# Optimization experiments

Measured on AMD Instinct MI355X. Metric: run time of the kernel, lower is better.

Reference implementation:

```python
import jax, jax.numpy as jnp
import numpy as np

NS, NW, E, DIN, OUT, H = 100_000, 400_000, 500_000, 64, 64, 4


def setup_inputs() -> dict:
    key = jax.random.key(0)
    ks = jax.random.split(key, 26)
    s = 1.0 / np.sqrt(DIN)
    sg = 1.0 / np.sqrt(OUT)
    inp = {
        "x_sites": jax.random.normal(ks[0], (NS, DIN), jnp.float32),
        "x_wells": jax.random.normal(ks[1], (NW, DIN), jnp.float32),
        "edge_sw_src": jax.random.randint(ks[2], (E,), 0, NS, jnp.int32),
        "edge_sw_dst": jax.random.randint(ks[3], (E,), 0, NW, jnp.int32),
        "edge_ws_src": jax.random.randint(ks[4], (E,), 0, NW, jnp.int32),
        "edge_ws_dst": jax.random.randint(ks[5], (E,), 0, NS, jnp.int32),
        # GAT ('pfas_sites','distance','gw_wells'), heads=4, concat=False
        "W_sw": jax.random.normal(ks[6], (DIN, H * OUT), jnp.float32) * s,
        "att_src_sw": jax.random.normal(ks[7], (H, OUT), jnp.float32) * sg,
        "att_dst_sw": jax.random.normal(ks[8], (H, OUT), jnp.float32) * sg,
        "b_sw": jnp.zeros((OUT,), jnp.float32),
        # SAGE ('gw_wells','distance','pfas_sites')
        "Wl_ws": jax.random.normal(ks[9], (DIN, OUT), jnp.float32) * s,
        "bl_ws": jnp.zeros((OUT,), jnp.float32),
        "Wr_ws": jax.random.normal(ks[10], (DIN, OUT), jnp.float32) * s,
        # GAT ('pfas_sites','self_loop','pfas_sites'), add_self_loops=True -> identity edges
        "W_ss": jax.random.normal(ks[11], (DIN, H * OUT), jnp.float32) * s,
        "att_src_ss": jax.random.normal(ks[12], (H, OUT), jnp.float32) * sg,
        "att_dst_ss": jax.random.normal(ks[13], (H, OUT), jnp.float32) * sg,
        "b_ss": jnp.zeros((OUT,), jnp.float32),
        # SAGE ('gw_wells','self_loop','gw_wells') with identity edges
        "Wl_ww": jax.random.normal(ks[14], (DIN, OUT), jnp.float32) * s,
        "bl_ww": jnp.zeros((OUT,), jnp.float32),
        "Wr_ww": jax.random.normal(ks[15], (DIN, OUT), jnp.float32) * s,
        # output heads
        "Wg": jax.random.normal(ks[16], (OUT, 1), jnp.float32) * sg,
        "bg": jnp.zeros((1,), jnp.float32),
        "Wsit": jax.random.normal(ks[17], (OUT, 1), jnp.float32) * sg,
        "bsit": jnp.zeros((1,), jnp.float32),
    }
    return inp


def _gat(x_src, x_dst, src, dst, W, a_src, a_dst, b, n_dst):
    """PyG GATConv, concat=False (mean over heads), negative_slope=0.2."""
    h, c = a_src.shape
    xs = (x_src @ W).reshape(-1, h, c)  # [Ns,H,C]
    xd = (x_dst @ W).reshape(-1, h, c)  # [Nd,H,C]
    al_s = jnp.einsum("nhc,hc->nh", xs, a_src)
    al_d = jnp.einsum("nhc,hc->nh", xd, a_dst)
    e = jax.nn.leaky_relu(al_s[src] + al_d[dst], 0.2)  # [E,H]
    m = jax.ops.segment_max(e, dst, num_segments=n_dst)
    ex = jnp.exp(e - m[dst])
    denom = jax.ops.segment_sum(ex, dst, num_segments=n_dst)
    alpha = ex / denom[dst]  # edge-softmax per dst node
    msg = xs[src] * alpha[:, :, None]  # [E,H,C] dominant intermediate
    out = jax.ops.segment_sum(msg, dst, num_segments=n_dst)
    return out.mean(axis=1) + b


def _sage(x_src, x_dst, src, dst, Wl, bl, Wr, n_dst):
    """PyG SAGEConv, mean aggregation, root_weight=True."""
    ssum = jax.ops.segment_sum(x_src[src], dst, num_segments=n_dst)
    cnt = jax.ops.segment_sum(jnp.ones((src.shape[0],), x_src.dtype), dst, num_segments=n_dst)
    mean = ssum / jnp.maximum(cnt, 1.0)[:, None]  # empty neighborhood -> 0 (PyG mean scatter)
    return mean @ Wl + bl + x_dst @ Wr


def reference(x_sites, x_wells, edge_sw_src, edge_sw_dst, edge_ws_src, edge_ws_dst,
              W_sw, att_src_sw, att_dst_sw, b_sw, Wl_ws, bl_ws, Wr_ws,
              W_ss, att_src_ss, att_dst_ss, b_ss, Wl_ww, bl_ww, Wr_ww,
              Wg, bg, Wsit, bsit):
    # relation 1: GAT sites -> wells
    gw = _gat(x_sites, x_wells, edge_sw_src, edge_sw_dst, W_sw, att_src_sw, att_dst_sw, b_sw, NW)
    # relation 4: SAGE self-loop on wells; identity edges -> mean == x itself
    gw = gw + (x_wells @ Wl_ww + bl_ww + x_wells @ Wr_ww)  # HeteroConv aggr='sum'
    # relation 2: SAGE wells -> sites
    si = _sage(x_wells, x_sites, edge_ws_src, edge_ws_dst, Wl_ws, bl_ws, Wr_ws, NS)
    # relation 3: GAT self-loop on sites (add_self_loops=True -> identity edge set);
    # softmax over a single self edge is 1, so output = mean over heads of lin(x) + bias
    si = si + (x_sites @ W_ss).reshape(NS, H, OUT).mean(axis=1) + b_ss
    # post: relu -> dropout (eval mode: identity) -> linear -> leaky_relu(0.01)
    gw = jax.nn.relu(gw)
    si = jax.nn.relu(si)
    o_gw = jax.nn.leaky_relu(gw @ Wg + bg, 0.01)   # [NW, 1]
    o_si = jax.nn.leaky_relu(si @ Wsit + bsit, 0.01)  # [NS, 1]
    return o_gw, o_si
```

## Files before the change

### kernel.cpp

```cpp
#include <hip/hip_runtime.h>

#define NS_ 100000
#define NW_ 400000
#define NE_ 500000
#define EPB 2048

typedef float f32x4_t __attribute__((ext_vector_type(4)));
typedef unsigned u32x4_t __attribute__((ext_vector_type(4)));

__device__ __forceinline__ float lrelu02(float x) { return x > 0.f ? x : 0.2f * x; }
__device__ __forceinline__ float bf2f(unsigned short u) {
    return __uint_as_float(((unsigned)u) << 16);
}
__device__ __forceinline__ unsigned short f2bf(float f) {
    unsigned u = __float_as_uint(f);
    u += 0x7FFFu + ((u >> 16) & 1u);
    return (unsigned short)(u >> 16);
}
__device__ __forceinline__ unsigned pk(float lo, float hi) {
    return (unsigned)f2bf(lo) | ((unsigned)f2bf(hi) << 16);
}
__device__ __forceinline__ void mfma_bf16(f32x4_t& acc, u32x4_t a, u32x4_t b) {
    asm volatile("v_mfma_f32_16x16x32_bf16 %0, %1, %2, %0" : "+v"(acc) : "v"(a), "v"(b));
}

__global__ void __launch_bounds__(256)
k_prep(const float* __restrict__ W_sw, const float* __restrict__ att_src,
       const float* __restrict__ att_dst,
       const float* __restrict__ Wl_ww, const float* __restrict__ Wr_ww,
       const float* __restrict__ Wl_ws, const float* __restrict__ Wr_ws,
       const float* __restrict__ W_ss,
       float* __restrict__ vd, float* __restrict__ vs,
       u32x4_t* __restrict__ fw, u32x4_t* __restrict__ fs,
       u32x4_t* __restrict__ fsp)
{
    const int tid = threadIdx.x;
    {
        int d = tid >> 2, h = tid & 3;
        const float4* wp = (const float4*)(W_sw + d * 256 + h * 64);
        const float4* ad = (const float4*)(att_dst + h * 64);
        const float4* as = (const float4*)(att_src + h * 64);
        float accd = 0.f, accs = 0.f;
#pragma unroll
        for (int c = 0; c < 16; ++c) {
            float4 wv = wp[c]; float4 dv = ad[c]; float4 sv = as[c];
            accd += wv.x * dv.x + wv.y * dv.y + wv.z * dv.z + wv.w * dv.w;
            accs += wv.x * sv.x + wv.y * sv.y + wv.z * sv.z + wv.w * sv.w;
        }
        vd[d * 4 + h] = accd;
        vs[d * 4 + h] = accs;
    }
    for (int idx = tid; idx < 512; idx += 256) {
        int f = idx >> 6, lane = idx & 63;
        int kc = f >> 2, ct = f & 3, q = lane >> 4, n = lane & 15;
        int c = ct * 16 + n;
        u32x4_t d;
#pragma unroll
        for (int i = 0; i < 4; ++i) {
            int k = kc * 32 + q * 8 + 2 * i;
            d[i] = pk(Wl_ww[k * 64 + c] + Wr_ww[k * 64 + c],
                      Wl_ww[(k + 1) * 64 + c] + Wr_ww[(k + 1) * 64 + c]);
        }
        fw[idx] = d;
    }
    for (int idx = tid; idx < 1024; idx += 256) {
        int f = idx >> 6, lane = idx & 63;
        int kc = f >> 2, ct = f & 3, q = lane >> 4, n = lane & 15;
        int c = ct * 16 + n;
        u32x4_t d;
#pragma unroll
        for (int i = 0; i < 4; ++i) {
            int k = kc * 32 + q * 8 + 2 * i;
            float lo, hi;
            if (k < 64) {
                lo = Wl_ws[k * 64 + c];
                hi = Wl_ws[(k + 1) * 64 + c];
            } else {
                int kk = k - 64;
                lo = Wr_ws[kk * 64 + c] + 0.25f * (W_ss[kk * 256 + c] + W_ss[kk * 256 + 64 + c] +
                                                   W_ss[kk * 256 + 128 + c] + W_ss[kk * 256 + 192 + c]);
                hi = Wr_ws[(kk + 1) * 64 + c] + 0.25f * (W_ss[(kk + 1) * 256 + c] + W_ss[(kk + 1) * 256 + 64 + c] +
                                                         W_ss[(kk + 1) * 256 + 128 + c] + W_ss[(kk + 1) * 256 + 192 + c]);
            }
            d[i] = pk(lo, hi);
        }
        fs[idx] = d;
    }
    for (int idx = tid; idx < 2048; idx += 256) {
        int f = idx >> 6, lane = idx & 63;
        int kc = f >> 4, ct = f & 15, q = lane >> 4, n = lane & 15;
        int c = ct * 16 + n;
        u32x4_t d;
#pragma unroll
        for (int i = 0; i < 4; ++i) {
            int k = kc * 32 + q * 8 + 2 * i;
            d[i] = pk(W_sw[k * 256 + c], W_sw[(k + 1) * 256 + c]);
        }
        fsp[idx] = d;
    }
}

#define SP_PAD 264
__global__ void __launch_bounds__(256)
k_sites_pre(const float* __restrict__ x_sites, const u32x4_t* __restrict__ fsp,
            const float* __restrict__ vs, unsigned short* __restrict__ xs,
            float* __restrict__ al_s)
{
    __shared__ unsigned short stg[4][16 * SP_PAD];
    __shared__ float vsl[256];
    const int tid = threadIdx.x;
    vsl[tid] = vs[tid];
    __syncthreads();
    const int wave = __builtin_amdgcn_readfirstlane(tid >> 6);
    const int lane = tid & 63, q = lane >> 4, n = lane & 15;
    const int sbase = blockIdx.x * 64 + wave * 16;
    const int srow = min(sbase + n, NS_ - 1);
    const float* xr = x_sites + (size_t)srow * 64 + q * 8;
    float4 x0 = *(const float4*)(xr);
    float4 x1 = *(const float4*)(xr + 4);
    float4 x2 = *(const float4*)(xr + 32);
    float4 x3 = *(const float4*)(xr + 36);
    u32x4_t am0 = { pk(x0.x, x0.y), pk(x0.z, x0.w), pk(x1.x, x1.y), pk(x1.z, x1.w) };
    u32x4_t am1 = { pk(x2.x, x2.y), pk(x2.z, x2.w), pk(x3.x, x3.y), pk(x3.z, x3.w) };
    float pa[4];
#pragma unroll
    for (int h = 0; h < 4; ++h) {
        const float* v0 = &vsl[(q * 8) * 4 + h];
        const float* v1 = &vsl[(32 + q * 8) * 4 + h];
        pa[h] = x0.x * v0[0]  + x0.y * v0[4]  + x0.z * v0[8]  + x0.w * v0[12]
              + x1.x * v0[16] + x1.y * v0[20] + x1.z * v0[24] + x1.w * v0[28]
              + x2.x * v1[0]  + x2.y * v1[4]  + x2.z * v1[8]  + x2.w * v1[12]
              + x3.x * v1[16] + x3.y * v1[20] + x3.z * v1[24] + x3.w * v1[28];
    }
#pragma unroll
    for (int h = 0; h < 4; ++h) {
        pa[h] += __shfl_xor(pa[h], 16, 64);
        pa[h] += __shfl_xor(pa[h], 32, 64);
    }
    if (q == 0 && sbase + n < NS_)
        *(float4*)(al_s + (size_t)(sbase + n) * 4) = make_float4(pa[0], pa[1], pa[2], pa[3]);

    f32x4_t acc[16];
#pragma unroll
    for (int ct = 0; ct < 16; ++ct) acc[ct] = (f32x4_t){0, 0, 0, 0};
    asm volatile("s_nop 3" : "+v"(am0), "+v"(am1));
#pragma unroll
    for (int ct = 0; ct < 16; ++ct) mfma_bf16(acc[ct], am0, fsp[ct * 64 + lane]);
#pragma unroll
    for (int ct = 0; ct < 16; ++ct) mfma_bf16(acc[ct], am1, fsp[(16 + ct) * 64 + lane]);
    asm volatile("s_nop 7\n\ts_nop 7" ::: "memory");
    unsigned short* ss = &stg[wave][0];
#pragma unroll
    for (int ct = 0; ct < 16; ++ct)
#pragma unroll
        for (int reg = 0; reg < 4; ++reg)
            ss[(q * 4 + reg) * SP_PAD + ct * 16 + n] = f2bf(acc[ct][reg]);
    __builtin_amdgcn_s_waitcnt(0);
#pragma unroll
    for (int i = 0; i < 8; ++i) {
        int g = i * 64 + lane;
        int r = g >> 5, c = g & 31;
        if (sbase + r < NS_) {
            u32x4_t v = *(const u32x4_t*)(ss + r * SP_PAD + c * 8);
            *(u32x4_t*)(xs + (size_t)(sbase + r) * 256 + c * 8) = v;
        }
    }
}

__global__ void __launch_bounds__(256)
k_hist2(const int* __restrict__ d1, int* __restrict__ h1,
        const int* __restrict__ d2, int* __restrict__ h2)
{
    int e = blockIdx.x * 256 + threadIdx.x;
    if (e >= NE_) return;
    if (blockIdx.y == 0) atomicAdd(&h1[d1[e]], 1);
    else                 atomicAdd(&h2[d2[e]], 1);
}

__global__ void __launch_bounds__(256)
k_scan1_2(const int* __restrict__ h1, int n1, int* __restrict__ b1, int nb1,
          const int* __restrict__ h2, int n2, int* __restrict__ b2)
{
    __shared__ int red[256];
    const int tid = threadIdx.x;
    const int bx = blockIdx.x;
    const int* hist; int n; int* bsum; int blk;
    if (bx < nb1) { hist = h1; n = n1; bsum = b1; blk = bx; }
    else          { hist = h2; n = n2; bsum = b2; blk = bx - nb1; }
    int base = blk * EPB + tid * 8;
    int s = 0;
#pragma unroll
    for (int i = 0; i < 8; ++i) { int idx = base + i; if (idx < n) s += hist[idx]; }
    red[tid] = s;
    __syncthreads();
    for (int off = 128; off > 0; off >>= 1) {
        if (tid < off) red[tid] += red[tid + off];
        __syncthreads();
    }
    if (tid == 0) bsum[blk] = red[0];
}

__global__ void __launch_bounds__(256)
k_scan2_2(int* __restrict__ b1, int nb1, int* __restrict__ b2, int nb2)
{
    __shared__ int sh[256];
    const int tid = threadIdx.x;
    int* bsum = blockIdx.x == 0 ? b1 : b2;
    int nb = blockIdx.x == 0 ? nb1 : nb2;
    sh[tid] = (tid < nb) ? bsum[tid] : 0;
    __syncthreads();
    for (int off = 1; off < 256; off <<= 1) {
        int u = (tid >= off) ? sh[tid - off] : 0;
        __syncthreads();
        sh[tid] += u;
        __syncthreads();
    }
    if (tid < nb) bsum[tid] = (tid == 0) ? 0 : sh[tid - 1];
}

__global__ void __launch_bounds__(256)
k_scan3_2(const int* __restrict__ h1, int n1, const int* __restrict__ b1,
          int* __restrict__ rp1, int* __restrict__ cu1, int nb1,
          const int* __restrict__ h2, int n2, const int* __restrict__ b2,
          int* __restrict__ rp2, int* __restrict__ cu2)
{
    __shared__ int tsum[256];
    const int tid = threadIdx.x;
    const int bx = blockIdx.x;
    const int* hist; int n; const int* bsum; int* rowptr; int* cursor; int blk;
    if (bx < nb1) { hist = h1; n = n1; bsum = b1; rowptr = rp1; cursor = cu1; blk = bx; }
    else          { hist = h2; n = n2; bsum = b2; rowptr = rp2; cursor = cu2; blk = bx - nb1; }
    int base = blk * EPB + tid * 8;
    int v[8]; int s = 0;
#pragma unroll
    for (int i = 0; i < 8; ++i) {
        int idx = base + i;
        v[i] = (idx < n) ? hist[idx] : 0;
        s += v[i];
    }
    tsum[tid] = s;
    __syncthreads();
    for (int off = 1; off < 256; off <<= 1) {
        int u = (tid >= off) ? tsum[tid - off] : 0;
        __syncthreads();
        tsum[tid] += u;
        __syncthreads();
    }
    int texcl = tsum[tid] - s;
    int run = bsum[blk] + texcl;
#pragma unroll
    for (int i = 0; i < 8; ++i) {
        int idx = base + i;
        if (idx < n) { rowptr[idx] = run; cursor[idx] = run; run += v[i]; }
    }
    if (blk == 0 && tid == 0) rowptr[n] = NE_;
}

__global__ void __launch_bounds__(256)
k_scatter2(const int* __restrict__ s1, const int* __restrict__ d1,
           int* __restrict__ c1, int* __restrict__ o1,
           const int* __restrict__ s2, const int* __restrict__ d2,
           int* __restrict__ c2, int* __restrict__ o2)
{
    int e = blockIdx.x * 256 + threadIdx.x;
    if (e >= NE_) return;
    if (blockIdx.y == 0) { int p = atomicAdd(&c1[d1[e]], 1); o1[p] = s1[e]; }
    else                 { int p = atomicAdd(&c2[d2[e]], 1); o2[p] = s2[e]; }
}

__global__ void __launch_bounds__(256)
k_gat_wells(const float* __restrict__ x_wells, const float* __restrict__ vd,
            const int* __restrict__ rowptr, const int* __restrict__ csr_src,
            const float* __restrict__ al_s, const unsigned short* __restrict__ xs,
            const float* __restrict__ b_sw, const float* __restrict__ bl_ww,
            const u32x4_t* __restrict__ fw, const float* __restrict__ Wg,
            const float* __restrict__ bg, float* __restrict__ out)
{
    __shared__ float vdl[16][17];
    __shared__ float xw[16][68];
    __shared__ float dl[16][68];
    __shared__ float biasl[64];
    __shared__ float wgl[64];
    __shared__ float res[16];
    const int tid = threadIdx.x;
    vdl[tid >> 4][tid & 15] = vd[tid];
    if (tid < 64) { biasl[tid] = b_sw[tid] + bl_ww[tid]; wgl[tid] = Wg[tid]; }
    __syncthreads();
    const int wl = tid >> 4, p = tid & 15;
    const int w = blockIdx.x * 16 + wl;
    float h0, h1, h2, h3;
    {
        float4 xv = *(const float4*)(x_wells + (size_t)w * 64 + 4 * p);
        *(float4*)&xw[wl][4 * p] = xv;
        const float* vp = vdl[p];
        h0 = xv.x * vp[0] + xv.y * vp[4] + xv.z * vp[8]  + xv.w * vp[12];
        h1 = xv.x * vp[1] + xv.y * vp[5] + xv.z * vp[9]  + xv.w * vp[13];
        h2 = xv.x * vp[2] + xv.y * vp[6] + xv.z * vp[10] + xv.w * vp[14];
        h3 = xv.x * vp[3] + xv.y * vp[7] + xv.z * vp[11] + xv.w * vp[15];
    }
#pragma unroll
    for (int off = 1; off < 16; off <<= 1) {
        h0 += __shfl_xor(h0, off, 64);
        h1 += __shfl_xor(h1, off, 64);
        h2 += __shfl_xor(h2, off, 64);
        h3 += __shfl_xor(h3, off, 64);
    }
    const int r0 = rowptr[w], r1 = rowptr[w + 1];
    float den0 = 0, den1 = 0, den2 = 0, den3 = 0;
    float n0[4] = {0, 0, 0, 0}, n1[4] = {0, 0, 0, 0};
    float n2[4] = {0, 0, 0, 0}, n3[4] = {0, 0, 0, 0};
    for (int j = r0; j < r1; ++j) {
        int s = csr_src[j];
        float4 as = ((const float4*)al_s)[s];
        float e0 = __expf(lrelu02(as.x + h0));
        float e1 = __expf(lrelu02(as.y + h1));
        float e2 = __expf(lrelu02(as.z + h2));
        float e3 = __expf(lrelu02(as.w + h3));
        den0 += e0; den1 += e1; den2 += e2; den3 += e3;
        const unsigned short* xr = xs + (size_t)s * 256 + 4 * p;
        ushort4 u0 = *(const ushort4*)(xr);
        ushort4 u1 = *(const ushort4*)(xr + 64);
        ushort4 u2 = *(const ushort4*)(xr + 128);
        ushort4 u3 = *(const ushort4*)(xr + 192);
        n0[0] += e0 * bf2f(u0.x); n0[1] += e0 * bf2f(u0.y); n0[2] += e0 * bf2f(u0.z); n0[3] += e0 * bf2f(u0.w);
        n1[0] += e1 * bf2f(u1.x); n1[1] += e1 * bf2f(u1.y); n1[2] += e1 * bf2f(u1.z); n1[3] += e1 * bf2f(u1.w);
        n2[0] += e2 * bf2f(u2.x); n2[1] += e2 * bf2f(u2.y); n2[2] += e2 * bf2f(u2.z); n2[3] += e2 * bf2f(u2.w);
        n3[0] += e3 * bf2f(u3.x); n3[1] += e3 * bf2f(u3.y); n3[2] += e3 * bf2f(u3.z); n3[3] += e3 * bf2f(u3.w);
    }
    const int c0 = 4 * p;
    float tmsg[4];
    if (r1 > r0) {
        float i0 = 0.25f / den0, i1 = 0.25f / den1, i2 = 0.25f / den2, i3 = 0.25f / den3;
#pragma unroll
        for (int i = 0; i < 4; ++i)
            tmsg[i] = n0[i] * i0 + n1[i] * i1 + n2[i] * i2 + n3[i] * i3 + biasl[c0 + i];
    } else {
#pragma unroll
        for (int i = 0; i < 4; ++i) tmsg[i] = biasl[c0 + i];
    }
    __syncthreads();
    const int wave = __builtin_amdgcn_readfirstlane(tid >> 6);
    const int lane = tid & 63, q = lane >> 4, n = lane & 15;
    u32x4_t a0, a1;
#pragma unroll
    for (int i = 0; i < 4; ++i) {
        a0[i] = pk(xw[n][q * 8 + 2 * i],      xw[n][q * 8 + 2 * i + 1]);
        a1[i] = pk(xw[n][32 + q * 8 + 2 * i], xw[n][32 + q * 8 + 2 * i + 1]);
    }
    f32x4_t acc = {0, 0, 0, 0};
    asm volatile("s_nop 3" : "+v"(a0), "+v"(a1), "+v"(acc));
    mfma_bf16(acc, a0, fw[wave * 64 + lane]);
    mfma_bf16(acc, a1, fw[(4 + wave) * 64 + lane]);
    asm volatile("s_nop 7\n\ts_nop 7" : "+v"(acc));
#pragma unroll
    for (int reg = 0; reg < 4; ++reg)
        dl[q * 4 + reg][wave * 16 + n] = acc[reg];
    __syncthreads();
    float4 dv = *(const float4*)&dl[wl][c0];
    float t0 = tmsg[0] + dv.x;
    float t1 = tmsg[1] + dv.y;
    float t2 = tmsg[2] + dv.z;
    float t3 = tmsg[3] + dv.w;
    float pr = fmaxf(t0, 0.f) * wgl[c0] + fmaxf(t1, 0.f) * wgl[c0 + 1] +
               fmaxf(t2, 0.f) * wgl[c0 + 2] + fmaxf(t3, 0.f) * wgl[c0 + 3];
    pr += __shfl_xor(pr, 1, 64);
    pr += __shfl_xor(pr, 2, 64);
    pr += __shfl_xor(pr, 4, 64);
    pr += __shfl_xor(pr, 8, 64);
    if (p == 0) res[wl] = pr + bg[0];
    __syncthreads();
    if (tid < 16) {
        float v = res[tid];
        out[blockIdx.x * 16 + tid] = v > 0.f ? v : 0.01f * v;
    }
}

__global__ void __launch_bounds__(256)
k_sage_sites(const float* __restrict__ x_sites, const float* __restrict__ x_wells,
             const int* __restrict__ rowptr, const int* __restrict__ csr_src,
             const u32x4_t* __restrict__ fs, const float* __restrict__ bl_ws,
             const float* __restrict__ b_ss, const float* __restrict__ Wsit,
             const float* __restrict__ bsit, float* __restrict__ out)
{
    __shared__ float mnL[16][68];
    __shared__ float xL[16][68];
    __shared__ float dl[16][68];
    __shared__ float biasl[64];
    __shared__ float wsl[64];
    __shared__ float res[16];
    const int tid = threadIdx.x;
    if (tid < 64) { biasl[tid] = bl_ws[tid] + b_ss[tid]; wsl[tid] = Wsit[tid]; }
    const int sl = tid >> 4, p = tid & 15;
    const int s = blockIdx.x * 16 + sl;
    const int r0 = rowptr[s], r1 = rowptr[s + 1];
    float4 m4 = {0.f, 0.f, 0.f, 0.f};
    for (int j = r0; j < r1; ++j) {
        int wsrc = csr_src[j];
        float4 xv = ((const float4*)(x_wells + (size_t)wsrc * 64))[p];
        m4.x += xv.x; m4.y += xv.y; m4.z += xv.z; m4.w += xv.w;
    }
    if (r1 > r0) {
        float rc = 1.f / (float)(r1 - r0);
        m4.x *= rc; m4.y *= rc; m4.z *= rc; m4.w *= rc;
    }
    *(float4*)&mnL[sl][4 * p] = m4;
    {
        float4 xv = *(const float4*)(x_sites + (size_t)s * 64 + 4 * p);
        *(float4*)&xL[sl][4 * p] = xv;
    }
    __syncthreads();
    const int wave = __builtin_amdgcn_readfirstlane(tid >> 6);
    const int lane = tid & 63, q = lane >> 4, n = lane & 15;
    u32x4_t am0, am1, ax0, ax1;
#pragma unroll
    for (int i = 0; i < 4; ++i) {
        am0[i] = pk(mnL[n][q * 8 + 2 * i],      mnL[n][q * 8 + 2 * i + 1]);
        am1[i] = pk(mnL[n][32 + q * 8 + 2 * i], mnL[n][32 + q * 8 + 2 * i + 1]);
        ax0[i] = pk(xL[n][q * 8 + 2 * i],       xL[n][q * 8 + 2 * i + 1]);
        ax1[i] = pk(xL[n][32 + q * 8 + 2 * i],  xL[n][32 + q * 8 + 2 * i + 1]);
    }
    f32x4_t acc = {0, 0, 0, 0};
    asm volatile("s_nop 3" : "+v"(am0), "+v"(am1), "+v"(ax0), "+v"(ax1), "+v"(acc));
    mfma_bf16(acc, am0, fs[wave * 64 + lane]);
    mfma_bf16(acc, am1, fs[(4 + wave) * 64 + lane]);
    mfma_bf16(acc, ax0, fs[(8 + wave) * 64 + lane]);
    mfma_bf16(acc, ax1, fs[(12 + wave) * 64 + lane]);
    asm volatile("s_nop 7\n\ts_nop 7" : "+v"(acc));
#pragma unroll
    for (int reg = 0; reg < 4; ++reg)
        dl[q * 4 + reg][wave * 16 + n] = acc[reg];
    __syncthreads();
    const int c0 = 4 * p;
    float4 dv = *(const float4*)&dl[sl][c0];
    float t0 = dv.x + biasl[c0];
    float t1 = dv.y + biasl[c0 + 1];
    float t2 = dv.z + biasl[c0 + 2];
    float t3 = dv.w + biasl[c0 + 3];
    float pr = fmaxf(t0, 0.f) * wsl[c0] + fmaxf(t1, 0.f) * wsl[c0 + 1] +
               fmaxf(t2, 0.f) * wsl[c0 + 2] + fmaxf(t3, 0.f) * wsl[c0 + 3];
    pr += __shfl_xor(pr, 1, 64);
    pr += __shfl_xor(pr, 2, 64);
    pr += __shfl_xor(pr, 4, 64);
    pr += __shfl_xor(pr, 8, 64);
    if (p == 0) res[sl] = pr + bsit[0];
    __syncthreads();
    if (tid < 16) {
        float v = res[tid];
        out[(size_t)NW_ + blockIdx.x * 16 + tid] = v > 0.f ? v : 0.01f * v;
    }
}

extern "C" void kernel_launch(void* const* d_in, const int* in_sizes, int n_in,
                              void* d_out, int out_size, void* d_ws, size_t ws_size,
                              hipStream_t stream)
{
    const float* x_sites    = (const float*)d_in[0];
    const float* x_wells    = (const float*)d_in[1];
    const int*   e_sw_src   = (const int*)d_in[2];
    const int*   e_sw_dst   = (const int*)d_in[3];
    const int*   e_ws_src   = (const int*)d_in[4];
    const int*   e_ws_dst   = (const int*)d_in[5];
    const float* W_sw       = (const float*)d_in[6];
    const float* att_src_sw = (const float*)d_in[7];
    const float* att_dst_sw = (const float*)d_in[8];
    const float* b_sw       = (const float*)d_in[9];
    const float* Wl_ws      = (const float*)d_in[10];
    const float* bl_ws      = (const float*)d_in[11];
    const float* Wr_ws      = (const float*)d_in[12];
    const float* W_ss       = (const float*)d_in[13];
    const float* b_ss       = (const float*)d_in[16];
    const float* Wl_ww      = (const float*)d_in[17];
    const float* bl_ww      = (const float*)d_in[18];
    const float* Wr_ww      = (const float*)d_in[19];
    const float* Wg         = (const float*)d_in[20];
    const float* bg         = (const float*)d_in[21];
    const float* Wsit       = (const float*)d_in[22];
    const float* bsit       = (const float*)d_in[23];
    float* out = (float*)d_out;

    unsigned short* xs = (unsigned short*)d_ws;
    float* al_s = (float*)(xs + (size_t)NS_ * 256);
    float* vd   = al_s + (size_t)NS_ * 4;
    float* vs   = vd + 256;
    u32x4_t* fw = (u32x4_t*)(vs + 256);
    u32x4_t* fs = fw + 512;
    u32x4_t* fsp= fs + 1024;
    int* ip     = (int*)(fsp + 2048);
    int* h_sw   = ip;
    int* h_ws   = h_sw + NW_;
    int* rp_sw  = h_ws + NS_;
    int* cur_sw = rp_sw + NW_ + 4;
    int* csr_sw = cur_sw + NW_;
    int* bs_sw  = csr_sw + NE_;
    int* rp_ws  = bs_sw + 256;
    int* cur_ws = rp_ws + NS_ + 4;
    int* csr_ws = cur_ws + NS_;
    int* bs_ws  = csr_ws + NE_;

    hipMemsetAsync(h_sw, 0, (size_t)(NW_ + NS_) * sizeof(int), stream);

    const int egrid = (NE_ + 255) / 256;
    const int nb_sw = (NW_ + EPB - 1) / EPB;
    const int nb_ws = (NS_ + EPB - 1) / EPB;

    hipLaunchKernelGGL(k_hist2, dim3(egrid, 2), dim3(256), 0, stream,
                       e_sw_dst, h_sw, e_ws_dst, h_ws);
    hipLaunchKernelGGL(k_scan1_2, dim3(nb_sw + nb_ws), dim3(256), 0, stream,
                       h_sw, NW_, bs_sw, nb_sw, h_ws, NS_, bs_ws);
    hipLaunchKernelGGL(k_scan2_2, dim3(2), dim3(256), 0, stream,
                       bs_sw, nb_sw, bs_ws, nb_ws);
    hipLaunchKernelGGL(k_scan3_2, dim3(nb_sw + nb_ws), dim3(256), 0, stream,
                       h_sw, NW_, bs_sw, rp_sw, cur_sw, nb_sw,
                       h_ws, NS_, bs_ws, rp_ws, cur_ws);
    hipLaunchKernelGGL(k_scatter2, dim3(egrid, 2), dim3(256), 0, stream,
                       e_sw_src, e_sw_dst, cur_sw, csr_sw,
                       e_ws_src, e_ws_dst, cur_ws, csr_ws);

    hipLaunchKernelGGL(k_prep, dim3(1), dim3(256), 0, stream,
                       W_sw, att_src_sw, att_dst_sw, Wl_ww, Wr_ww, Wl_ws, Wr_ws, W_ss,
                       vd, vs, fw, fs, fsp);
    hipLaunchKernelGGL(k_sites_pre, dim3((NS_ + 63) / 64), dim3(256), 0, stream,
                       x_sites, fsp, vs, xs, al_s);

    hipLaunchKernelGGL(k_gat_wells, dim3(NW_ / 16), dim3(256), 0, stream,
                       x_wells, vd, rp_sw, csr_sw, al_s, xs, b_sw, bl_ww,
                       fw, Wg, bg, out);
    hipLaunchKernelGGL(k_sage_sites, dim3(NS_ / 16), dim3(256), 0, stream,
                       x_sites, x_wells, rp_ws, csr_ws, fs, bl_ws, b_ss,
                       Wsit, bsit, out);
}
```

Baseline: 468.5 us.

## Inline first two well neighbors in per-node descriptor and pack staging as bf16

Replaces the wells rowptr/cursor pair with an int4 descriptor per well (start, degree, first two source ids) filled during scatter. The GAT kernel can then issue its first two neighbor gathers up front without the dependent csr_src load. The per-site bf16 features are permuted on store so each lane reads two contiguous 16-byte vectors instead of four 8-byte ones. The LDS staging in both consumer kernels holds packed bf16, so the MFMA operand is one vector load. It costs an extra per-well counter memset, a larger descriptor array and extra scatter writes.

```diff
diff --git a/kernel.cpp b/kernel.cpp
--- a/kernel.cpp
+++ b/kernel.cpp
@@ -12,6 +12,8 @@
 __device__ __forceinline__ float bf2f(unsigned short u) {
     return __uint_as_float(((unsigned)u) << 16);
 }
+__device__ __forceinline__ float lo16(unsigned u) { return __uint_as_float(u << 16); }
+__device__ __forceinline__ float hi16(unsigned u) { return __uint_as_float(u & 0xFFFF0000u); }
 __device__ __forceinline__ unsigned short f2bf(float f) {
     unsigned u = __float_as_uint(f);
     u += 0x7FFFu + ((u >> 16) & 1u);
@@ -150,11 +152,14 @@
     for (int ct = 0; ct < 16; ++ct) mfma_bf16(acc[ct], am1, fsp[(16 + ct) * 64 + lane]);
     asm volatile("s_nop 7\n\ts_nop 7" ::: "memory");
     unsigned short* ss = &stg[wave][0];
-#pragma unroll
-    for (int ct = 0; ct < 16; ++ct)
+    const int pbase = ((n >> 2) * 16) + (n & 3);
+#pragma unroll
+    for (int ct = 0; ct < 16; ++ct) {
+        const int cidx = pbase + (ct & 3) * 64 + (ct >> 2) * 4;
 #pragma unroll
         for (int reg = 0; reg < 4; ++reg)
-            ss[(q * 4 + reg) * SP_PAD + ct * 16 + n] = f2bf(acc[ct][reg]);
+            ss[(q * 4 + reg) * SP_PAD + cidx] = f2bf(acc[ct][reg]);
+    }
     __builtin_amdgcn_s_waitcnt(0);
 #pragma unroll
     for (int i = 0; i < 8; ++i) {
@@ -220,16 +225,16 @@
 
 __global__ void __launch_bounds__(256)
 k_scan3_2(const int* __restrict__ h1, int n1, const int* __restrict__ b1,
-          int* __restrict__ rp1, int* __restrict__ cu1, int nb1,
+          int4* __restrict__ desc, int nb1,
           const int* __restrict__ h2, int n2, const int* __restrict__ b2,
           int* __restrict__ rp2, int* __restrict__ cu2)
 {
     __shared__ int tsum[256];
     const int tid = threadIdx.x;
     const int bx = blockIdx.x;
-    const int* hist; int n; const int* bsum; int* rowptr; int* cursor; int blk;
-    if (bx < nb1) { hist = h1; n = n1; bsum = b1; rowptr = rp1; cursor = cu1; blk = bx; }
-    else          { hist = h2; n = n2; bsum = b2; rowptr = rp2; cursor = cu2; blk = bx - nb1; }
+    const int* hist; int n; const int* bsum; int blk; int wells;
+    if (bx < nb1) { hist = h1; n = n1; bsum = b1; blk = bx; wells = 1; }
+    else          { hist = h2; n = n2; bsum = b2; blk = bx - nb1; wells = 0; }
     int base = blk * EPB + tid * 8;
     int v[8]; int s = 0;
 #pragma unroll
@@ -248,36 +253,52 @@
     }
     int texcl = tsum[tid] - s;
     int run = bsum[blk] + texcl;
-#pragma unroll
-    for (int i = 0; i < 8; ++i) {
-        int idx = base + i;
-        if (idx < n) { rowptr[idx] = run; cursor[idx] = run; run += v[i]; }
-    }
-    if (blk == 0 && tid == 0) rowptr[n] = NE_;
+    if (wells) {
+#pragma unroll
+        for (int i = 0; i < 8; ++i) {
+            int idx = base + i;
+            if (idx < n) { desc[idx] = make_int4(run, v[i], 0, 0); run += v[i]; }
+        }
+    } else {
+#pragma unroll
+        for (int i = 0; i < 8; ++i) {
+            int idx = base + i;
+            if (idx < n) { rp2[idx] = run; cu2[idx] = run; run += v[i]; }
+        }
+        if (blk == 0 && tid == 0) rp2[n] = NE_;
+    }
 }
 
 __global__ void __launch_bounds__(256)
 k_scatter2(const int* __restrict__ s1, const int* __restrict__ d1,
-           int* __restrict__ c1, int* __restrict__ o1,
+           int* __restrict__ cnt0, int* __restrict__ desc_i, int* __restrict__ o1,
            const int* __restrict__ s2, const int* __restrict__ d2,
            int* __restrict__ c2, int* __restrict__ o2)
 {
     int e = blockIdx.x * 256 + threadIdx.x;
     if (e >= NE_) return;
-    if (blockIdx.y == 0) { int p = atomicAdd(&c1[d1[e]], 1); o1[p] = s1[e]; }
-    else                 { int p = atomicAdd(&c2[d2[e]], 1); o2[p] = s2[e]; }
+    if (blockIdx.y == 0) {
+        int d = d1[e], s = s1[e];
+        int pr = atomicAdd(&cnt0[d], 1);
+        int start = desc_i[4 * d];
+        o1[start + pr] = s;
+        if (pr < 2) desc_i[4 * d + 2 + pr] = s;
+    } else {
+        int p = atomicAdd(&c2[d2[e]], 1);
+        o2[p] = s2[e];
+    }
 }
 
 __global__ void __launch_bounds__(256)
 k_gat_wells(const float* __restrict__ x_wells, const float* __restrict__ vd,
-            const int* __restrict__ rowptr, const int* __restrict__ csr_src,
+            const int4* __restrict__ desc, const int* __restrict__ csr_src,
             const float* __restrict__ al_s, const unsigned short* __restrict__ xs,
             const float* __restrict__ b_sw, const float* __restrict__ bl_ww,
             const u32x4_t* __restrict__ fw, const float* __restrict__ Wg,
             const float* __restrict__ bg, float* __restrict__ out)
 {
     __shared__ float vdl[16][17];
-    __shared__ float xw[16][68];
+    __shared__ unsigned xwB[16][36];
     __shared__ float dl[16][68];
     __shared__ float biasl[64];
     __shared__ float wgl[64];
@@ -288,10 +309,24 @@
     __syncthreads();
     const int wl = tid >> 4, p = tid & 15;
     const int w = blockIdx.x * 16 + wl;
+    const int4 dsc = desc[w];
+    const int deg = dsc.y;
+    float4 as0 = ((const float4*)al_s)[dsc.z];
+    const unsigned short* x0p = xs + (size_t)dsc.z * 256 + p * 16;
+    u32x4_t va0 = *(const u32x4_t*)(x0p);
+    u32x4_t vb0 = *(const u32x4_t*)(x0p + 8);
+    float4 as1 = as0; u32x4_t va1 = va0, vb1 = vb0;
+    if (deg > 1) {
+        as1 = ((const float4*)al_s)[dsc.w];
+        const unsigned short* x1p = xs + (size_t)dsc.w * 256 + p * 16;
+        va1 = *(const u32x4_t*)(x1p);
+        vb1 = *(const u32x4_t*)(x1p + 8);
+    }
     float h0, h1, h2, h3;
     {
         float4 xv = *(const float4*)(x_wells + (size_t)w * 64 + 4 * p);
-        *(float4*)&xw[wl][4 * p] = xv;
+        xwB[wl][2 * p]     = pk(xv.x, xv.y);
+        xwB[wl][2 * p + 1] = pk(xv.z, xv.w);
         const float* vp = vdl[p];
         h0 = xv.x * vp[0] + xv.y * vp[4] + xv.z * vp[8]  + xv.w * vp[12];
         h1 = xv.x * vp[1] + xv.y * vp[5] + xv.z * vp[9]  + xv.w * vp[13];
@@ -305,31 +340,37 @@
         h2 += __shfl_xor(h2, off, 64);
         h3 += __shfl_xor(h3, off, 64);
     }
-    const int r0 = rowptr[w], r1 = rowptr[w + 1];
     float den0 = 0, den1 = 0, den2 = 0, den3 = 0;
     float n0[4] = {0, 0, 0, 0}, n1[4] = {0, 0, 0, 0};
     float n2[4] = {0, 0, 0, 0}, n3[4] = {0, 0, 0, 0};
-    for (int j = r0; j < r1; ++j) {
-        int s = csr_src[j];
-        float4 as = ((const float4*)al_s)[s];
+    auto acc_edge = [&](float4 as, u32x4_t va, u32x4_t vb) {
         float e0 = __expf(lrelu02(as.x + h0));
         float e1 = __expf(lrelu02(as.y + h1));
         float e2 = __expf(lrelu02(as.z + h2));
         float e3 = __expf(lrelu02(as.w + h3));
         den0 += e0; den1 += e1; den2 += e2; den3 += e3;
-        const unsigned short* xr = xs + (size_t)s * 256 + 4 * p;
-        ushort4 u0 = *(const ushort4*)(xr);
-        ushort4 u1 = *(const ushort4*)(xr + 64);
-        ushort4 u2 = *(const ushort4*)(xr + 128);
-        ushort4 u3 = *(const ushort4*)(xr + 192);
-        n0[0] += e0 * bf2f(u0.x); n0[1] += e0 * bf2f(u0.y); n0[2] += e0 * bf2f(u0.z); n0[3] += e0 * bf2f(u0.w);
-        n1[0] += e1 * bf2f(u1.x); n1[1] += e1 * bf2f(u1.y); n1[2] += e1 * bf2f(u1.z); n1[3] += e1 * bf2f(u1.w);
-        n2[0] += e2 * bf2f(u2.x); n2[1] += e2 * bf2f(u2.y); n2[2] += e2 * bf2f(u2.z); n2[3] += e2 * bf2f(u2.w);
-        n3[0] += e3 * bf2f(u3.x); n3[1] += e3 * bf2f(u3.y); n3[2] += e3 * bf2f(u3.z); n3[3] += e3 * bf2f(u3.w);
+        n0[0] += e0 * lo16(va[0]); n0[1] += e0 * hi16(va[0]);
+        n0[2] += e0 * lo16(va[1]); n0[3] += e0 * hi16(va[1]);
+        n1[0] += e1 * lo16(va[2]); n1[1] += e1 * hi16(va[2]);
+        n1[2] += e1 * lo16(va[3]); n1[3] += e1 * hi16(va[3]);
+        n2[0] += e2 * lo16(vb[0]); n2[1] += e2 * hi16(vb[0]);
+        n2[2] += e2 * lo16(vb[1]); n2[3] += e2 * hi16(vb[1]);
+        n3[0] += e3 * lo16(vb[2]); n3[1] += e3 * hi16(vb[2]);
+        n3[2] += e3 * lo16(vb[3]); n3[3] += e3 * hi16(vb[3]);
+    };
+    if (deg > 0) acc_edge(as0, va0, vb0);
+    if (deg > 1) acc_edge(as1, va1, vb1);
+    for (int j = 2; j < deg; ++j) {
+        int s = csr_src[dsc.x + j];
+        float4 as = ((const float4*)al_s)[s];
+        const unsigned short* xr = xs + (size_t)s * 256 + p * 16;
+        u32x4_t va = *(const u32x4_t*)(xr);
+        u32x4_t vb = *(const u32x4_t*)(xr + 8);
+        acc_edge(as, va, vb);
     }
     const int c0 = 4 * p;
     float tmsg[4];
-    if (r1 > r0) {
+    if (deg > 0) {
         float i0 = 0.25f / den0, i1 = 0.25f / den1, i2 = 0.25f / den2, i3 = 0.25f / den3;
 #pragma unroll
         for (int i = 0; i < 4; ++i)
@@ -341,16 +382,12 @@
     __syncthreads();
     const int wave = __builtin_amdgcn_readfirstlane(tid >> 6);
     const int lane = tid & 63, q = lane >> 4, n = lane & 15;
-    u32x4_t a0, a1;
-#pragma unroll
-    for (int i = 0; i < 4; ++i) {
-        a0[i] = pk(xw[n][q * 8 + 2 * i],      xw[n][q * 8 + 2 * i + 1]);
-        a1[i] = pk(xw[n][32 + q * 8 + 2 * i], xw[n][32 + q * 8 + 2 * i + 1]);
-    }
+    u32x4_t ax0 = *(const u32x4_t*)&xwB[n][q * 4];
+    u32x4_t ax1 = *(const u32x4_t*)&xwB[n][16 + q * 4];
     f32x4_t acc = {0, 0, 0, 0};
-    asm volatile("s_nop 3" : "+v"(a0), "+v"(a1), "+v"(acc));
-    mfma_bf16(acc, a0, fw[wave * 64 + lane]);
-    mfma_bf16(acc, a1, fw[(4 + wave) * 64 + lane]);
+    asm volatile("s_nop 3" : "+v"(ax0), "+v"(ax1), "+v"(acc));
+    mfma_bf16(acc, ax0, fw[wave * 64 + lane]);
+    mfma_bf16(acc, ax1, fw[(4 + wave) * 64 + lane]);
     asm volatile("s_nop 7\n\ts_nop 7" : "+v"(acc));
 #pragma unroll
     for (int reg = 0; reg < 4; ++reg)
@@ -382,8 +419,8 @@
              const float* __restrict__ b_ss, const float* __restrict__ Wsit,
              const float* __restrict__ bsit, float* __restrict__ out)
 {
-    __shared__ float mnL[16][68];
-    __shared__ float xL[16][68];
+    __shared__ unsigned mnB[16][36];
+    __shared__ unsigned xB[16][36];
     __shared__ float dl[16][68];
     __shared__ float biasl[64];
     __shared__ float wsl[64];
@@ -403,22 +440,20 @@
         float rc = 1.f / (float)(r1 - r0);
         m4.x *= rc; m4.y *= rc; m4.z *= rc; m4.w *= rc;
     }
-    *(float4*)&mnL[sl][4 * p] = m4;
+    mnB[sl][2 * p]     = pk(m4.x, m4.y);
+    mnB[sl][2 * p + 1] = pk(m4.z, m4.w);
     {
         float4 xv = *(const float4*)(x_sites + (size_t)s * 64 + 4 * p);
-        *(float4*)&xL[sl][4 * p] = xv;
+        xB[sl][2 * p]     = pk(xv.x, xv.y);
+        xB[sl][2 * p + 1] = pk(xv.z, xv.w);
     }
     __syncthreads();
     const int wave = __builtin_amdgcn_readfirstlane(tid >> 6);
     const int lane = tid & 63, q = lane >> 4, n = lane & 15;
-    u32x4_t am0, am1, ax0, ax1;
-#pragma unroll
-    for (int i = 0; i < 4; ++i) {
-        am0[i] = pk(mnL[n][q * 8 + 2 * i],      mnL[n][q * 8 + 2 * i + 1]);
-        am1[i] = pk(mnL[n][32 + q * 8 + 2 * i], mnL[n][32 + q * 8 + 2 * i + 1]);
-        ax0[i] = pk(xL[n][q * 8 + 2 * i],       xL[n][q * 8 + 2 * i + 1]);
-        ax1[i] = pk(xL[n][32 + q * 8 + 2 * i],  xL[n][32 + q * 8 + 2 * i + 1]);
-    }
+    u32x4_t am0 = *(const u32x4_t*)&mnB[n][q * 4];
+    u32x4_t am1 = *(const u32x4_t*)&mnB[n][16 + q * 4];
+    u32x4_t ax0 = *(const u32x4_t*)&xB[n][q * 4];
+    u32x4_t ax1 = *(const u32x4_t*)&xB[n][16 + q * 4];
     f32x4_t acc = {0, 0, 0, 0};
     asm volatile("s_nop 3" : "+v"(am0), "+v"(am1), "+v"(ax0), "+v"(ax1), "+v"(acc));
     mfma_bf16(acc, am0, fs[wave * 64 + lane]);
@@ -488,16 +523,16 @@
     int* ip     = (int*)(fsp + 2048);
     int* h_sw   = ip;
     int* h_ws   = h_sw + NW_;
-    int* rp_sw  = h_ws + NS_;
-    int* cur_sw = rp_sw + NW_ + 4;
-    int* csr_sw = cur_sw + NW_;
+    int* cnt0   = h_ws + NS_;
+    int* desc_i = cnt0 + NW_;
+    int* csr_sw = desc_i + 4 * (size_t)NW_;
     int* bs_sw  = csr_sw + NE_;
     int* rp_ws  = bs_sw + 256;
     int* cur_ws = rp_ws + NS_ + 4;
     int* csr_ws = cur_ws + NS_;
     int* bs_ws  = csr_ws + NE_;
 
-    hipMemsetAsync(h_sw, 0, (size_t)(NW_ + NS_) * sizeof(int), stream);
+    hipMemsetAsync(h_sw, 0, (size_t)(NW_ + NS_ + NW_) * sizeof(int), stream);
 
     const int egrid = (NE_ + 255) / 256;
     const int nb_sw = (NW_ + EPB - 1) / EPB;
@@ -510,10 +545,10 @@
     hipLaunchKernelGGL(k_scan2_2, dim3(2), dim3(256), 0, stream,
                        bs_sw, nb_sw, bs_ws, nb_ws);
     hipLaunchKernelGGL(k_scan3_2, dim3(nb_sw + nb_ws), dim3(256), 0, stream,
-                       h_sw, NW_, bs_sw, rp_sw, cur_sw, nb_sw,
+                       h_sw, NW_, bs_sw, (int4*)desc_i, nb_sw,
                        h_ws, NS_, bs_ws, rp_ws, cur_ws);
     hipLaunchKernelGGL(k_scatter2, dim3(egrid, 2), dim3(256), 0, stream,
-                       e_sw_src, e_sw_dst, cur_sw, csr_sw,
+                       e_sw_src, e_sw_dst, cnt0, desc_i, csr_sw,
                        e_ws_src, e_ws_dst, cur_ws, csr_ws);
 
     hipLaunchKernelGGL(k_prep, dim3(1), dim3(256), 0, stream,
@@ -523,8 +558,8 @@
                        x_sites, fsp, vs, xs, al_s);
 
     hipLaunchKernelGGL(k_gat_wells, dim3(NW_ / 16), dim3(256), 0, stream,
-                       x_wells, vd, rp_sw, csr_sw, al_s, xs, b_sw, bl_ww,
-                       fw, Wg, bg, out);
+                       x_wells, vd, (const int4*)desc_i, csr_sw, al_s, xs,
+                       b_sw, bl_ww, fw, Wg, bg, out);
     hipLaunchKernelGGL(k_sage_sites, dim3(NS_ / 16), dim3(256), 0, stream,
                        x_sites, x_wells, rp_ws, csr_ws, fs, bl_ws, b_ss,
                        Wsit, bsit, out);
```

New measurement: 478.9 us. +2.2%, slower.
